# Optimization experiments

Measured on AMD Instinct MI355X. Metric: run time of the kernel, lower is better.

## Reference

```python
import jax, jax.numpy as jnp
import numpy as np

H = 16  # num_heads


def setup_inputs() -> dict:
    key = jax.random.key(0)
    ks = jax.random.split(key, 8)
    B, S, d, L = 1, 2048, 1024, 8
    hd = d // H
    s = 0.02
    return {
        "x": jax.random.normal(ks[0], (B, S, d), jnp.float32),
        "past_values": jax.random.normal(ks[1], (L, B, H, S, hd), jnp.float32),
        "Wqkv": jax.random.normal(ks[2], (3 * d, d), jnp.float32) * s,
        "bqkv": jax.random.normal(ks[3], (3 * d,), jnp.float32) * s,
        "Wcol": jax.random.normal(ks[4], (d, d), jnp.float32) * s,
        "bcol": jax.random.normal(ks[5], (d,), jnp.float32) * s,
        "Wout": jax.random.normal(ks[6], (d, d), jnp.float32) * s,
        "bout": jax.random.normal(ks[7], (d,), jnp.float32) * s,
    }


def reference(x, past_values, Wqkv, bqkv, Wcol, bcol, Wout, bout):
    B, S, d = x.shape
    L = past_values.shape[0]
    hd = d // H
    scale = 1.0 / np.sqrt(hd).astype(np.float32)

    qkv = x @ Wqkv.T + bqkv                       # [B,S,3d]
    q, k, v = jnp.split(qkv, 3, axis=-1)

    def heads(t):                                  # [B,S,d] -> [B,H,S,hd]
        return t.reshape(B, S, H, hd).transpose(0, 2, 1, 3)

    q_row, k, v = heads(q), heads(k), heads(v)
    q_col = heads(x @ Wcol.T + bcol)

    # causal token scores [B,H,S,S]
    token_scores = jnp.einsum('bhqd,bhkd->bhqk', q_row, k) * scale
    causal = jnp.triu(jnp.ones((S, S), bool), 1)
    token_scores = jnp.where(causal, -jnp.inf, token_scores)

    # stack past values: torch stack(dim=3) -> [B,H,S,L,hd]; permute -> [B,S,L,H*hd]
    pv = past_values.transpose(1, 3, 0, 2, 4).reshape(B, S, L, d)
    ri = pv.reshape(B, S * L, d)
    mu = ri.mean(-1, keepdims=True)
    var = ri.var(-1, keepdims=True)
    ri = (ri - mu) / jnp.sqrt(var + 1e-5)          # F.layer_norm, no affine

    Wk, bk = Wqkv[d:2 * d], bqkv[d:2 * d]
    Wv, bv = Wqkv[2 * d:], bqkv[2 * d:]
    rk = (ri @ Wk.T + bk).reshape(B, S * L, H, hd).transpose(0, 2, 1, 3).reshape(B, H, S, L, hd)
    rv = (ri @ Wv.T + bv).reshape(B, S * L, H, hd).transpose(0, 2, 1, 3).reshape(B, H, S, L, hd)

    mem_scores = jnp.einsum('bhsd,bhsld->bhsl', q_col, rk) * scale  # [B,H,S,L]

    scores = jnp.concatenate([token_scores, mem_scores], axis=-1)   # [B,H,S,S+L]
    w = jax.nn.softmax(scores, axis=-1)
    tw, mw = w[..., :S], w[..., S:]

    ctx = jnp.einsum('bhqk,bhkd->bhqd', tw, v) + jnp.einsum('bhsl,bhsld->bhsd', mw, rv)
    out = ctx.transpose(0, 2, 1, 3).reshape(B, S, d)
    return out @ Wout.T + bout
```

## Files before the change

### kernel.cpp

```cpp
#include <hip/hip_runtime.h>
#include <math.h>

#define D   1024
#define H   16
#define HD  64
#define SEQ 2048
#define LL  8
#define SCALE 0.125f

typedef __attribute__((ext_vector_type(8))) __bf16 bf16x8;
typedef __attribute__((ext_vector_type(4))) float floatx4;
typedef __attribute__((ext_vector_type(8))) unsigned short ushort8;

__device__ inline unsigned short f32_to_bf16(float f) {
    unsigned int u = __builtin_bit_cast(unsigned int, f);
    u += 0x7FFF + ((u >> 16) & 1);
    return (unsigned short)(u >> 16);
}
__device__ inline float bf2f(unsigned short u) {
    unsigned int x = (unsigned int)u << 16;
    return __builtin_bit_cast(float, x);
}
__device__ inline void load_lds16(const void* g, void* l) {
    __builtin_amdgcn_global_load_lds(
        (__attribute__((address_space(1))) void*)g,
        (__attribute__((address_space(3))) void*)l, 16, 0, 0);
}

__device__ inline void xcd_swizzle(int& bx, int& by) {
    const int gx   = gridDim.x;
    const int lin  = blockIdx.y * gx + blockIdx.x;
    const int nblk = gx * gridDim.y;
    const int virt = (lin & 7) * (nblk >> 3) + (lin >> 3);
    bx = virt % gx;
    by = virt / gx;
}

#define NQ_X    524288
#define NQ_WQKV 786432
#define NQ_WC   262144
#define NQ_WO   262144
#define LN_BLK  16384
#define CVT_BLK 7168
#define PREP_GRID (LN_BLK + CVT_BLK + 4)

__global__ __launch_bounds__(256) void prep_kernel(
    const float* __restrict__ pv, const float* __restrict__ x,
    const float* __restrict__ Wqkv, const float* __restrict__ Wcol,
    const float* __restrict__ Wout, const float* __restrict__ bqkv,
    const float* __restrict__ bcol,
    unsigned short* __restrict__ ri, unsigned short* __restrict__ xb,
    unsigned short* __restrict__ W4b, unsigned short* __restrict__ Woutb,
    float* __restrict__ b4)
{
    const int b = blockIdx.x;
    const int t = threadIdx.x;
    if (b < LN_BLK) {
        const int r = b;
        const int s = r >> 3, l = r & 7;
        const int h = t >> 4, e = (t & 15) * 4;
        const size_t src = (size_t)l * (H * SEQ * HD) + (size_t)h * (SEQ * HD)
                         + (size_t)s * HD + e;
        float4 v = *(const float4*)(pv + src);
        float sum = v.x + v.y + v.z + v.w;
        float sq  = v.x * v.x + v.y * v.y + v.z * v.z + v.w * v.w;
#pragma unroll
        for (int off = 32; off; off >>= 1) {
            sum += __shfl_xor(sum, off);
            sq  += __shfl_xor(sq, off);
        }
        __shared__ float red[8];
        if ((t & 63) == 0) { red[(t >> 6) * 2] = sum; red[(t >> 6) * 2 + 1] = sq; }
        __syncthreads();
        sum = red[0] + red[2] + red[4] + red[6];
        sq  = red[1] + red[3] + red[5] + red[7];
        const float mean = sum * (1.f / 1024.f);
        const float var  = sq * (1.f / 1024.f) - mean * mean;
        const float rstd = rsqrtf(var + 1e-5f);
        ushort4 o;
        o.x = f32_to_bf16((v.x - mean) * rstd);
        o.y = f32_to_bf16((v.y - mean) * rstd);
        o.z = f32_to_bf16((v.z - mean) * rstd);
        o.w = f32_to_bf16((v.w - mean) * rstd);
        *(ushort4*)(ri + (size_t)r * D + t * 4) = o;
    } else if (b < LN_BLK + CVT_BLK) {
        const int i = (b - LN_BLK) * 256 + t;
        const float* src; unsigned short* dst; int off;
        if (i < NQ_X)                        { src = x;    dst = xb;    off = i; }
        else if (i < NQ_X + NQ_WQKV)         { src = Wqkv; dst = W4b;   off = i - NQ_X; }
        else if (i < NQ_X + NQ_WQKV + NQ_WC) {
            float4 v = ((const float4*)Wcol)[i - NQ_X - NQ_WQKV];
            ushort4 o;
            o.x = f32_to_bf16(v.x); o.y = f32_to_bf16(v.y);
            o.z = f32_to_bf16(v.z); o.w = f32_to_bf16(v.w);
            ((ushort4*)(W4b))[NQ_WQKV + (i - NQ_X - NQ_WQKV)] = o;
            return;
        }
        else                                 { src = Wout; dst = Woutb; off = i - NQ_X - NQ_WQKV - NQ_WC; }
        float4 v = ((const float4*)src)[off];
        ushort4 o;
        o.x = f32_to_bf16(v.x); o.y = f32_to_bf16(v.y);
        o.z = f32_to_bf16(v.z); o.w = f32_to_bf16(v.w);
        ((ushort4*)dst)[off] = o;
    } else {
        const int q = (b - LN_BLK - CVT_BLK) * 256 + t;
        float4 v = (q < 768) ? ((const float4*)bqkv)[q] : ((const float4*)bcol)[q - 768];
        ((float4*)b4)[q] = v;
    }
}

__global__ __launch_bounds__(256) void wkt_kernel(
    const float* __restrict__ Wqkv, unsigned short* __restrict__ WkT)
{
    const int h = blockIdx.x >> 4, ct = blockIdx.x & 15;
    const int c0 = ct * 64;
    const int t = threadIdx.x;
    __shared__ float tile[64][68];
    {
        const int e  = t >> 2;
        const int c4 = (t & 3) * 16;
        const float* src = Wqkv + (size_t)(D + h * HD + e) * D + c0 + c4;
#pragma unroll
        for (int j = 0; j < 4; j++) {
            float4 v = ((const float4*)src)[j];
            *(float4*)&tile[e][c4 + j * 4] = v;
        }
    }
    __syncthreads();
    {
        const int c  = t >> 2;
        const int e0 = (t & 3) * 16;
        ushort8 o0, o1;
#pragma unroll
        for (int j = 0; j < 8; j++) o0[j] = f32_to_bf16(tile[e0 + j][c]);
#pragma unroll
        for (int j = 0; j < 8; j++) o1[j] = f32_to_bf16(tile[e0 + 8 + j][c]);
        unsigned short* dst = WkT + (size_t)h * (D * HD) + (size_t)(c0 + c) * HD + e0;
        *(ushort8*)dst       = o0;
        *(ushort8*)(dst + 8) = o1;
    }
}

template <typename CT, bool HAS_BIAS>
__global__ __launch_bounds__(256) void gemm_bf16_kernel(
    const unsigned short* __restrict__ A, const unsigned short* __restrict__ W,
    const float* __restrict__ bias, CT* __restrict__ C,
    int K, int N, int lda, int ldw, int ldc,
    size_t zsA, size_t zsW, size_t zsC)
{
    A += (size_t)blockIdx.z * zsA;
    W += (size_t)blockIdx.z * zsW;
    C += (size_t)blockIdx.z * zsC;

    __shared__ unsigned short As[128 * 32];
    __shared__ unsigned short Ws[128 * 32];
    const int t    = threadIdx.x;
    const int wave = t >> 6, lane = t & 63;
    const int wm   = wave >> 1, wn = wave & 1;
    int bx, by;
    xcd_swizzle(bx, by);
    const int m0 = by * 128, n0 = bx * 128;

    floatx4 acc[4][4];
#pragma unroll
    for (int i = 0; i < 4; i++)
#pragma unroll
        for (int j = 0; j < 4; j++) acc[i][j] = (floatx4)0.f;

    const int lrow = lane >> 2;
    const int lcol = (lane & 3) * 8;
    const unsigned short* Ag = A + (size_t)(m0 + wave * 32 + lrow) * lda + lcol;
    const unsigned short* Wg = W + (size_t)(n0 + wave * 32 + lrow) * ldw + lcol;
    unsigned short* Asw = &As[wave * 32 * 32];
    unsigned short* Wsw = &Ws[wave * 32 * 32];
    const size_t rowskipA = (size_t)16 * lda;
    const size_t rowskipW = (size_t)16 * ldw;

    const int arow  = lane & 15;
    const int aquad = (lane >> 4) * 8;

    for (int k0 = 0; k0 < K; k0 += 32) {
        load_lds16(Ag + k0,             Asw);
        load_lds16(Ag + k0 + rowskipA,  Asw + 16 * 32);
        load_lds16(Wg + k0,             Wsw);
        load_lds16(Wg + k0 + rowskipW,  Wsw + 16 * 32);
        __syncthreads();

        bf16x8 af[4], wf[4];
#pragma unroll
        for (int mi = 0; mi < 4; mi++)
            af[mi] = *(const bf16x8*)&As[(wm * 64 + mi * 16 + arow) * 32 + aquad];
#pragma unroll
        for (int ni = 0; ni < 4; ni++)
            wf[ni] = *(const bf16x8*)&Ws[(wn * 64 + ni * 16 + arow) * 32 + aquad];
#pragma unroll
        for (int mi = 0; mi < 4; mi++)
#pragma unroll
            for (int ni = 0; ni < 4; ni++)
                acc[mi][ni] = __builtin_amdgcn_mfma_f32_16x16x32_bf16(
                    af[mi], wf[ni], acc[mi][ni], 0, 0, 0);
        __syncthreads();
    }

    const int crow = (lane >> 4) * 4, ccol = lane & 15;
#pragma unroll
    for (int mi = 0; mi < 4; mi++) {
#pragma unroll
        for (int ni = 0; ni < 4; ni++) {
            const int gm = m0 + wm * 64 + mi * 16 + crow;
            const int gn = n0 + wn * 64 + ni * 16 + ccol;
            float bb = 0.f;
            if constexpr (HAS_BIAS) bb = bias[gn];
#pragma unroll
            for (int r = 0; r < 4; r++) {
                float v = acc[mi][ni][r] + bb;
                if constexpr (sizeof(CT) == 2)
                    C[(size_t)(gm + r) * ldc + gn] = (CT)f32_to_bf16(v);
                else
                    C[(size_t)(gm + r) * ldc + gn] = v;
            }
        }
    }
}

#define RI_STRIDE 1032

__global__ __launch_bounds__(256) void memsc_kernel(
    const unsigned short* __restrict__ U, const unsigned short* __restrict__ ri,
    const unsigned short* __restrict__ qkv4, const float* __restrict__ bqkv,
    float* __restrict__ scores)
{
    const int s = blockIdx.x;
    const int t = threadIdx.x;
    __shared__ unsigned short riS[LL * RI_STRIDE];
    __shared__ float qbS[H];
    {
        const unsigned short* src = ri + (size_t)s * (LL * D);
#pragma unroll
        for (int j = 0; j < 4; j++) {
            const int off = (j * 256 + t) * 8;
            const int l = off >> 10, c = off & 1023;
            ushort8 v = *(const ushort8*)(src + off);
            *(ushort8*)&riS[l * RI_STRIDE + c] = v;
        }
    }
    {
        const int h = t >> 4, sub = t & 15;
        const unsigned short* qc = qkv4 + (size_t)s * 4096 + 3 * D + h * HD + sub * 4;
        const float* bk = bqkv + D + h * HD + sub * 4;
        float acc = 0.f;
#pragma unroll
        for (int j = 0; j < 4; j++) acc += bf2f(qc[j]) * bk[j];
#pragma unroll
        for (int off = 1; off < 16; off <<= 1) acc += __shfl_xor(acc, off);
        if (sub == 0) qbS[h] = acc;
    }
    __syncthreads();
    const int p = t >> 1, half = t & 1;
    const int h = p >> 3, l = p & 7;
    const unsigned short* Up = U + ((size_t)h * SEQ + s) * D + half * 512;
    const unsigned short* rp = &riS[l * RI_STRIDE + half * 512];
    float acc = 0.f;
#pragma unroll 4
    for (int j = 0; j < 64; j++) {
        ushort8 u = *(const ushort8*)(Up + j * 8);
        ushort8 r = *(const ushort8*)(rp + j * 8);
#pragma unroll
        for (int k = 0; k < 8; k++) acc += bf2f(u[k]) * bf2f(r[k]);
    }
    acc += __shfl_xor(acc, 1);
    if (half == 0)
        scores[((size_t)s * H + h) * LL + l] = (acc + qbS[h]) * SCALE;
}

__global__ __launch_bounds__(256) void attn_split_kernel(
    const unsigned short* __restrict__ qkv4,
    const float* __restrict__ mem_scores, float* __restrict__ memP,
    float* __restrict__ Opart, float2* __restrict__ mlpart)
{
    const int t    = threadIdx.x;
    const int w    = t >> 6, lane = t & 63;
    const int lrow = lane & 15;
    const int lk   = (lane >> 4) * 8;
    const int rrow = (lane >> 4) * 4;
    const int lin  = blockIdx.x;
    const int hsp  = lin & 63, g = lin >> 6;
    const int h    = hsp >> 2, s = hsp & 3;
    const int qt   = 31 - g;
    const int q0   = qt * 64;
    const int n    = qt + 1;
    const int lo   = (s * n) >> 2, hi = ((s + 1) * n) >> 2;
    const int part = (h * 32 + qt) * 4 + s;

    __shared__ unsigned short Ks[64 * 72];
    __shared__ unsigned short Vt[64 * 72];
    __shared__ unsigned short Pb[64 * 72];
    __shared__ float row_m[64], row_l[64];
    __shared__ float mem_mm[64], mem_alpha[64], mem_suml[64];

    bf16x8 qreg[2];
#pragma unroll
    for (int kst = 0; kst < 2; kst++)
        qreg[kst] = *(const bf16x8*)(qkv4 + (size_t)(q0 + w * 16 + lrow) * 4096
                                     + h * HD + kst * 32 + lk);

    bf16x8 kr[2];
    ushort8 va, vb;
    const int vpr = t & 31, veg = t >> 5;

    float m_i[4], l_i[4];
    floatx4 Oacc[4];
#pragma unroll
    for (int r = 0; r < 4; r++) { m_i[r] = -1e30f; l_i[r] = 0.f; }
#pragma unroll
    for (int et = 0; et < 4; et++) Oacc[et] = (floatx4)0.f;

    const int krow = (t >> 3);
    const int kcol = (t & 7) * 8;

    if (lo < hi) {
        const int j0 = lo * 64;
#pragma unroll
        for (int p = 0; p < 2; p++)
            kr[p] = *(const bf16x8*)(qkv4 + (size_t)(j0 + p * 32 + krow) * 4096
                                     + D + h * HD + kcol);
        const unsigned short* v0 =
            qkv4 + (size_t)(j0 + 2 * vpr) * 4096 + 2 * D + h * HD + veg * 8;
        va = *(const ushort8*)v0;
        vb = *(const ushort8*)(v0 + 4096);
#pragma unroll
        for (int p = 0; p < 2; p++)
            *(bf16x8*)&Ks[(p * 32 + krow) * 72 + kcol] = kr[p];
#pragma unroll
        for (int j = 0; j < 8; j++) {
            unsigned int pk = (unsigned int)va[j] | ((unsigned int)vb[j] << 16);
            *(unsigned int*)&Vt[(veg * 8 + j) * 72 + 2 * vpr] = pk;
        }
        __syncthreads();
    }

    for (int jt = lo; jt < hi; jt++) {
        const int j0 = jt * 64;
        const bool pf = (jt + 1 < hi);
        if (pf) {
            const int j0n = (jt + 1) * 64;
#pragma unroll
            for (int p = 0; p < 2; p++)
                kr[p] = *(const bf16x8*)(qkv4 + (size_t)(j0n + p * 32 + krow) * 4096
                                         + D + h * HD + kcol);
            const unsigned short* v0 =
                qkv4 + (size_t)(j0n + 2 * vpr) * 4096 + 2 * D + h * HD + veg * 8;
            va = *(const ushort8*)v0;
            vb = *(const ushort8*)(v0 + 4096);
        }

        floatx4 S[4];
#pragma unroll
        for (int nt = 0; nt < 4; nt++) S[nt] = (floatx4)0.f;
        __builtin_amdgcn_s_setprio(1);
#pragma unroll
        for (int kst = 0; kst < 2; kst++) {
#pragma unroll
            for (int nt = 0; nt < 4; nt++) {
                bf16x8 bk = *(const bf16x8*)&Ks[(nt * 16 + lrow) * 72 + kst * 32 + lk];
                S[nt] = __builtin_amdgcn_mfma_f32_16x16x32_bf16(qreg[kst], bk, S[nt], 0, 0, 0);
            }
        }
        __builtin_amdgcn_s_setprio(0);

        if (j0 != q0) {
#pragma unroll
            for (int r = 0; r < 4; r++) {
                float sc[4];
#pragma unroll
                for (int nt = 0; nt < 4; nt++) sc[nt] = S[nt][r] * SCALE;
                float mx = fmaxf(fmaxf(sc[0], sc[1]), fmaxf(sc[2], sc[3]));
#pragma unroll
                for (int off = 1; off < 16; off <<= 1)
                    mx = fmaxf(mx, __shfl_xor(mx, off));
                const bool keep = __all(mx <= m_i[r] + 8.f);
                const float newm = keep ? m_i[r] : fmaxf(m_i[r], mx);
                float ps = 0.f;
#pragma unroll
                for (int nt = 0; nt < 4; nt++) {
                    float pe = __expf(sc[nt] - newm);
                    ps += pe;
                    Pb[(w * 16 + rrow + r) * 72 + nt * 16 + lrow] = f32_to_bf16(pe);
                }
#pragma unroll
                for (int off = 1; off < 16; off <<= 1)
                    ps += __shfl_xor(ps, off);
                if (keep) {
                    l_i[r] += ps;
                } else {
                    const float alpha = __expf(m_i[r] - newm);
                    m_i[r] = newm;
                    l_i[r] = l_i[r] * alpha + ps;
#pragma unroll
                    for (int et = 0; et < 4; et++) Oacc[et][r] *= alpha;
                }
            }
        } else {
#pragma unroll
            for (int r = 0; r < 4; r++) {
                const int qg = q0 + w * 16 + rrow + r;
                float sc[4];
                float mx = -1e30f;
#pragma unroll
                for (int nt = 0; nt < 4; nt++) {
                    sc[nt] = S[nt][r] * SCALE;
                    if (j0 + nt * 16 + lrow > qg) sc[nt] = -1e30f;
                    mx = fmaxf(mx, sc[nt]);
                }
#pragma unroll
                for (int off = 1; off < 16; off <<= 1)
                    mx = fmaxf(mx, __shfl_xor(mx, off));
                const float newm  = fmaxf(m_i[r], mx);
                const float alpha = __expf(m_i[r] - newm);
                m_i[r] = newm;
                float ps = 0.f;
#pragma unroll
                for (int nt = 0; nt < 4; nt++) {
                    float pe = __expf(sc[nt] - newm);
                    ps += pe;
                    Pb[(w * 16 + rrow + r) * 72 + nt * 16 + lrow] = f32_to_bf16(pe);
                }
#pragma unroll
                for (int off = 1; off < 16; off <<= 1)
                    ps += __shfl_xor(ps, off);
                l_i[r] = l_i[r] * alpha + ps;
#pragma unroll
                for (int et = 0; et < 4; et++) Oacc[et][r] *= alpha;
            }
        }

        __builtin_amdgcn_s_setprio(1);
#pragma unroll
        for (int kst = 0; kst < 2; kst++) {
            bf16x8 ap = *(const bf16x8*)&Pb[(w * 16 + lrow) * 72 + kst * 32 + lk];
#pragma unroll
            for (int et = 0; et < 4; et++) {
                bf16x8 bv = *(const bf16x8*)&Vt[(et * 16 + lrow) * 72 + kst * 32 + lk];
                Oacc[et] = __builtin_amdgcn_mfma_f32_16x16x32_bf16(ap, bv, Oacc[et], 0, 0, 0);
            }
        }
        __builtin_amdgcn_s_setprio(0);

        if (pf) {
            __syncthreads();
#pragma unroll
            for (int p = 0; p < 2; p++)
                *(bf16x8*)&Ks[(p * 32 + krow) * 72 + kcol] = kr[p];
#pragma unroll
            for (int j = 0; j < 8; j++) {
                unsigned int pk = (unsigned int)va[j] | ((unsigned int)vb[j] << 16);
                *(unsigned int*)&Vt[(veg * 8 + j) * 72 + 2 * vpr] = pk;
            }
            __syncthreads();
        }
    }

    if (s != 0) {
#pragma unroll
        for (int r = 0; r < 4; r++) {
            const int ql = w * 16 + rrow + r;
            if (lrow == 0) mlpart[(size_t)part * 64 + ql] = make_float2(m_i[r], l_i[r]);
#pragma unroll
            for (int et = 0; et < 4; et++)
                Opart[((size_t)part * 64 + ql) * 64 + et * 16 + lrow] = Oacc[et][r];
        }
        return;
    }

#pragma unroll
    for (int r = 0; r < 4; r++) {
        const int ql = w * 16 + rrow + r;
        if (lrow == 0) { row_m[ql] = m_i[r]; row_l[ql] = l_i[r]; }
    }
    __syncthreads();

    if (t < 64) {
        const int qi = t, qg = q0 + qi;
        const float* msp = mem_scores + ((size_t)qg * H + h) * LL;
        float ms[LL];
#pragma unroll
        for (int l = 0; l < LL; l++) ms[l] = msp[l];
        const float mo = row_m[qi];
        float mm = mo;
#pragma unroll
        for (int l = 0; l < LL; l++) mm = fmaxf(mm, ms[l]);
        const float alpha = __expf(mo - mm);
        float suml = 0.f;
        float* mp = memP + ((size_t)qg * H + h) * LL;
#pragma unroll
        for (int l = 0; l < LL; l++) {
            float pe = __expf(ms[l] - mm);
            suml += pe;
            mp[l] = pe;
        }
        mem_mm[qi] = mm; mem_alpha[qi] = alpha; mem_suml[qi] = suml;
    }
    __syncthreads();

#pragma unroll
    for (int r = 0; r < 4; r++) {
        const int ql = w * 16 + rrow + r;
        const float alpha = mem_alpha[ql];
        if (lrow == 0)
            mlpart[(size_t)part * 64 + ql] =
                make_float2(mem_mm[ql], l_i[r] * alpha + mem_suml[ql]);
#pragma unroll
        for (int et = 0; et < 4; et++)
            Opart[((size_t)part * 64 + ql) * 64 + et * 16 + lrow] = Oacc[et][r] * alpha;
    }
}

__global__ __launch_bounds__(256) void attn_merge_kernel(
    const float* __restrict__ Opart, const float2* __restrict__ mlpart,
    const float* __restrict__ memP,
    float* __restrict__ tok, float* __restrict__ mwf, float* __restrict__ Pmem)
{
    const int blk = blockIdx.x;
    const int h = blk >> 5, qt = blk & 31;
    const int q0 = qt * 64;
    const int t = threadIdx.x, tx = t & 15, ty = t >> 4;
    const size_t pb = (size_t)blk * 4;
#pragma unroll
    for (int i = 0; i < 4; i++) {
        const int qi = ty * 4 + i, qg = q0 + qi;
        float2 ml[4];
#pragma unroll
        for (int ps = 0; ps < 4; ps++) ml[ps] = mlpart[(pb + ps) * 64 + qi];
        float M = ml[0].x;
#pragma unroll
        for (int ps = 1; ps < 4; ps++) M = fmaxf(M, ml[ps].x);
        float f[4], L = 0.f;
#pragma unroll
        for (int ps = 0; ps < 4; ps++) { f[ps] = __expf(ml[ps].x - M); L += ml[ps].y * f[ps]; }
        const float rl = 1.f / L;
        float4 o = make_float4(0.f, 0.f, 0.f, 0.f);
#pragma unroll
        for (int ps = 0; ps < 4; ps++) {
            const float fs = f[ps] * rl;
            float4 op = *(const float4*)&Opart[((pb + ps) * 64 + qi) * 64 + tx * 4];
            o.x += op.x * fs; o.y += op.y * fs; o.z += op.z * fs; o.w += op.w * fs;
        }
        *(float4*)&tok[(size_t)qg * D + h * HD + tx * 4] = o;
        if (tx == 0) {
            const float w0 = f[0] * rl;
            const float* mp = memP + ((size_t)qg * H + h) * LL;
            float* mw = mwf + ((size_t)qg * H + h) * LL;
            float psum = 0.f;
#pragma unroll
            for (int l = 0; l < LL; l++) { float v = mp[l] * w0; mw[l] = v; psum += v; }
            Pmem[(size_t)qg * H + h] = psum;
        }
    }
}

__global__ __launch_bounds__(256) void rbar_kernel(
    const float* __restrict__ mwf, const unsigned short* __restrict__ ri,
    unsigned short* __restrict__ rbar)
{
    const int s = blockIdx.x, t = threadIdx.x;
    __shared__ unsigned short riS[LL * D];
    __shared__ float wS[H * LL];
    {
        const unsigned short* src = ri + (size_t)s * (LL * D);
#pragma unroll
        for (int j = 0; j < 4; j++) {
            const int off = (j * 256 + t) * 8;
            *(ushort8*)&riS[off] = *(const ushort8*)(src + off);
        }
    }
    if (t < H * LL) wS[t] = mwf[(size_t)s * (H * LL) + t];
    __syncthreads();
    const int c4 = t * 4;
#pragma unroll
    for (int hh = 0; hh < H; hh++) {
        float v0 = 0.f, v1 = 0.f, v2 = 0.f, v3 = 0.f;
#pragma unroll
        for (int l = 0; l < LL; l++) {
            const float wv = wS[hh * LL + l];
            ushort4 rr = *(const ushort4*)&riS[l * D + c4];
            v0 += wv * bf2f(rr.x); v1 += wv * bf2f(rr.y);
            v2 += wv * bf2f(rr.z); v3 += wv * bf2f(rr.w);
        }
        ushort4 o;
        o.x = f32_to_bf16(v0); o.y = f32_to_bf16(v1);
        o.z = f32_to_bf16(v2); o.w = f32_to_bf16(v3);
        *(ushort4*)(rbar + ((size_t)hh * SEQ + s) * D + c4) = o;
    }
}

__global__ __launch_bounds__(256) void gemm_ctx_kernel(
    const unsigned short* __restrict__ rbar, const unsigned short* __restrict__ W4,
    const float* __restrict__ bqkv, const float* __restrict__ Pmem,
    const float* __restrict__ tok, unsigned short* __restrict__ ctx)
{
    const int mt = blockIdx.x;
    const int h  = blockIdx.y;
    const unsigned short* A  = rbar + (size_t)h * SEQ * D + (size_t)mt * 128 * D;
    const unsigned short* Wv = W4 + (size_t)(2 * D + h * HD) * D;
    const float* bv = bqkv + 2 * D + h * HD;

    __shared__ unsigned short As[128 * 32];
    __shared__ unsigned short Ws[64 * 32];
    const int t    = threadIdx.x;
    const int wave = t >> 6, lane = t & 63;

    floatx4 acc[2][4];
#pragma unroll
    for (int i = 0; i < 2; i++)
#pragma unroll
        for (int j = 0; j < 4; j++) acc[i][j] = (floatx4)0.f;

    const int lrow = lane >> 2;
    const int lcol = (lane & 3) * 8;
    const unsigned short* Ag = A  + (size_t)(wave * 32 + lrow) * D + lcol;
    const unsigned short* Wg = Wv + (size_t)(wave * 32 + lrow) * D + lcol;
    unsigned short* Asw = &As[wave * 32 * 32];
    unsigned short* Wsw = &Ws[wave * 32 * 32];
    const size_t rowskip = (size_t)16 * D;

    const int arow  = lane & 15;
    const int aquad = (lane >> 4) * 8;

    for (int k0 = 0; k0 < D; k0 += 32) {
        load_lds16(Ag + k0,           Asw);
        load_lds16(Ag + k0 + rowskip, Asw + 16 * 32);
        if (wave < 2) {
            load_lds16(Wg + k0,           Wsw);
            load_lds16(Wg + k0 + rowskip, Wsw + 16 * 32);
        }
        __syncthreads();

        bf16x8 af[2], wf[4];
#pragma unroll
        for (int mi = 0; mi < 2; mi++)
            af[mi] = *(const bf16x8*)&As[(wave * 32 + mi * 16 + arow) * 32 + aquad];
#pragma unroll
        for (int ni = 0; ni < 4; ni++)
            wf[ni] = *(const bf16x8*)&Ws[(ni * 16 + arow) * 32 + aquad];
#pragma unroll
        for (int mi = 0; mi < 2; mi++)
#pragma unroll
            for (int ni = 0; ni < 4; ni++)
                acc[mi][ni] = __builtin_amdgcn_mfma_f32_16x16x32_bf16(
                    af[mi], wf[ni], acc[mi][ni], 0, 0, 0);
        __syncthreads();
    }

    const int crow = (lane >> 4) * 4, ccol = lane & 15;
#pragma unroll
    for (int mi = 0; mi < 2; mi++) {
#pragma unroll
        for (int ni = 0; ni < 4; ni++) {
            const int e  = ni * 16 + ccol;
            const float bb = bv[e];
#pragma unroll
            for (int r = 0; r < 4; r++) {
                const int grow = mt * 128 + wave * 32 + mi * 16 + crow + r;
                float v = acc[mi][ni][r] + bb * Pmem[(size_t)grow * H + h]
                          + tok[(size_t)grow * D + h * HD + e];
                ctx[(size_t)grow * D + h * HD + e] = f32_to_bf16(v);
            }
        }
    }
}

extern "C" void kernel_launch(void* const* d_in, const int* in_sizes, int n_in,
                              void* d_out, int out_size, void* d_ws, size_t ws_size,
                              hipStream_t stream)
{
    const float* x    = (const float*)d_in[0];
    const float* pv   = (const float*)d_in[1];
    const float* Wqkv = (const float*)d_in[2];
    const float* bqkv = (const float*)d_in[3];
    const float* Wcol = (const float*)d_in[4];
    const float* bcol = (const float*)d_in[5];
    const float* Wout = (const float*)d_in[6];
    const float* bout = (const float*)d_in[7];
    float* out = (float*)d_out;

    char* p = (char*)d_ws;
    unsigned short* x_bf    = (unsigned short*)p; p += (size_t)2048 * 1024 * 2;
    unsigned short* W4_bf   = (unsigned short*)p; p += (size_t)4096 * 1024 * 2;
    unsigned short* Wout_bf = (unsigned short*)p; p += (size_t)1024 * 1024 * 2;
    float*          b4      = (float*)p;          p += (size_t)4096 * 4;
    unsigned short* ri_bf   = (unsigned short*)p; p += (size_t)16384 * 1024 * 2;
    unsigned short* qkv4_bf = (unsigned short*)p; p += (size_t)2048 * 4096 * 2;
    unsigned short* WkT_bf  = (unsigned short*)p; p += (size_t)16 * 1024 * 64 * 2;
    float*          scores  = (float*)p;          p += (size_t)2048 * 16 * 8 * 4;
    float*          memP    = (float*)p;          p += (size_t)2048 * 16 * 8 * 4;
    float*          mwf     = (float*)p;          p += (size_t)2048 * 16 * 8 * 4;
    float*          Pmem    = (float*)p;          p += (size_t)2048 * 16 * 4;
    float*          tok     = (float*)p;          p += (size_t)2048 * 1024 * 4;
    unsigned short* ctx_bf  = (unsigned short*)p; p += (size_t)2048 * 1024 * 2;
    float*          Opart   = (float*)p;          p += (size_t)2048 * 64 * 64 * 4;
    float2*         mlpart  = (float2*)p;         p += (size_t)2048 * 64 * 8;
    unsigned short* Urb     = (unsigned short*)p; p += (size_t)16 * 2048 * 1024 * 2;

    prep_kernel<<<PREP_GRID, 256, 0, stream>>>(pv, x, Wqkv, Wcol, Wout, bqkv, bcol,
                                               ri_bf, x_bf, W4_bf, Wout_bf, b4);
    wkt_kernel<<<256, 256, 0, stream>>>(Wqkv, WkT_bf);
    gemm_bf16_kernel<unsigned short, true><<<dim3(32, 16, 1), 256, 0, stream>>>(
        x_bf, W4_bf, b4, qkv4_bf, 1024, 4096, 1024, 1024, 4096, 0, 0, 0);
    gemm_bf16_kernel<unsigned short, false><<<dim3(8, 16, 16), 256, 0, stream>>>(
        qkv4_bf + 3 * D, WkT_bf, nullptr, Urb, 64, 1024, 4096, 64, 1024,
        (size_t)HD, (size_t)D * HD, (size_t)SEQ * D);
    memsc_kernel<<<2048, 256, 0, stream>>>(Urb, ri_bf, qkv4_bf, bqkv, scores);
    attn_split_kernel<<<2048, 256, 0, stream>>>(qkv4_bf, scores, memP, Opart, mlpart);
    attn_merge_kernel<<<512, 256, 0, stream>>>(Opart, mlpart, memP, tok, mwf, Pmem);
    rbar_kernel<<<2048, 256, 0, stream>>>(mwf, ri_bf, Urb);
    gemm_ctx_kernel<<<dim3(16, 16), 256, 0, stream>>>(Urb, W4_bf, bqkv, Pmem, tok, ctx_bf);
    gemm_bf16_kernel<float, true><<<dim3(8, 16, 1), 256, 0, stream>>>(
        ctx_bf, Wout_bf, bout, out, 1024, 1024, 1024, 1024, 1024, 0, 0, 0);
}
```

Before: 339.1 us.

## Pre-transpose V and read K/V directly from global in split attention

Adds a kernel that writes V transposed per head into a workspace buffer. The split-attention kernel then reads K and V MFMA operands straight from global memory instead of staging them through shared memory with barriers. Only a per-wave P buffer stays in shared memory. The scale is folded into Q before the bf16 rounding, which slightly changes numerics. The memory-score softmax merge moves from the split kernel into the merge kernel, and the block-to-(head, split) mapping and launch bounds change to raise occupancy. The trade is more uncached global traffic and an extra launch in exchange for no LDS staging and no block-wide syncs.

```diff
diff --git a/kernel.cpp b/kernel.cpp
--- a/kernel.cpp
+++ b/kernel.cpp
@@ -141,6 +141,35 @@
     }
 }
 
+__global__ __launch_bounds__(256) void vtr_kernel(
+    const unsigned short* __restrict__ qkv4, unsigned short* __restrict__ VT)
+{
+    const int h = blockIdx.x & 15, kt = blockIdx.x >> 4;
+    const int t = threadIdx.x;
+    __shared__ unsigned short Vt[64][264];
+    const int pr = t & 31, eg = t >> 5;
+#pragma unroll
+    for (int sub = 0; sub < 4; sub++) {
+        const int j0 = kt * 256 + sub * 64;
+        const unsigned short* v0 = qkv4 + (size_t)(j0 + 2 * pr) * 4096 + 2 * D + h * HD + eg * 8;
+        ushort8 va = *(const ushort8*)v0;
+        ushort8 vb = *(const ushort8*)(v0 + 4096);
+#pragma unroll
+        for (int j = 0; j < 8; j++) {
+            unsigned int pk = (unsigned int)va[j] | ((unsigned int)vb[j] << 16);
+            *(unsigned int*)&Vt[eg * 8 + j][sub * 64 + 2 * pr] = pk;
+        }
+    }
+    __syncthreads();
+#pragma unroll
+    for (int it = 0; it < 8; it++) {
+        const int idx = it * 256 + t;
+        const int e = idx >> 5, ch = idx & 31;
+        ushort8 v = *(const ushort8*)&Vt[e][ch * 8];
+        *(ushort8*)(VT + (size_t)h * (HD * SEQ) + (size_t)e * SEQ + kt * 256 + ch * 8) = v;
+    }
+}
+
 template <typename CT, bool HAS_BIAS>
 __global__ __launch_bounds__(256) void gemm_bf16_kernel(
     const unsigned short* __restrict__ A, const unsigned short* __restrict__ W,
@@ -273,9 +302,8 @@
         scores[((size_t)s * H + h) * LL + l] = (acc + qbS[h]) * SCALE;
 }
 
-__global__ __launch_bounds__(256) void attn_split_kernel(
-    const unsigned short* __restrict__ qkv4,
-    const float* __restrict__ mem_scores, float* __restrict__ memP,
+__global__ __launch_bounds__(256, 4) void attn_split_kernel(
+    const unsigned short* __restrict__ qkv4, const unsigned short* __restrict__ VT,
     float* __restrict__ Opart, float2* __restrict__ mlpart)
 {
     const int t    = threadIdx.x;
@@ -285,28 +313,29 @@
     const int rrow = (lane >> 4) * 4;
     const int lin  = blockIdx.x;
     const int hsp  = lin & 63, g = lin >> 6;
-    const int h    = hsp >> 2, s = hsp & 3;
+    const int s    = hsp >> 4, h = hsp & 15;
     const int qt   = 31 - g;
     const int q0   = qt * 64;
     const int n    = qt + 1;
     const int lo   = (s * n) >> 2, hi = ((s + 1) * n) >> 2;
     const int part = (h * 32 + qt) * 4 + s;
 
-    __shared__ unsigned short Ks[64 * 72];
-    __shared__ unsigned short Vt[64 * 72];
-    __shared__ unsigned short Pb[64 * 72];
-    __shared__ float row_m[64], row_l[64];
-    __shared__ float mem_mm[64], mem_alpha[64], mem_suml[64];
+    __shared__ unsigned short Pb[4][16 * 72];
+    unsigned short* Pw = Pb[w];
 
     bf16x8 qreg[2];
 #pragma unroll
-    for (int kst = 0; kst < 2; kst++)
-        qreg[kst] = *(const bf16x8*)(qkv4 + (size_t)(q0 + w * 16 + lrow) * 4096
-                                     + h * HD + kst * 32 + lk);
-
-    bf16x8 kr[2];
-    ushort8 va, vb;
-    const int vpr = t & 31, veg = t >> 5;
+    for (int kst = 0; kst < 2; kst++) {
+        ushort8 qu = *(const ushort8*)(qkv4 + (size_t)(q0 + w * 16 + lrow) * 4096
+                                       + h * HD + kst * 32 + lk);
+        ushort8 qs;
+#pragma unroll
+        for (int j = 0; j < 8; j++) qs[j] = f32_to_bf16(bf2f(qu[j]) * SCALE);
+        qreg[kst] = __builtin_bit_cast(bf16x8, qs);
+    }
+
+    const unsigned short* Kbase = qkv4 + D + h * HD;
+    const unsigned short* Vbase = VT + (size_t)h * (HD * SEQ);
 
     float m_i[4], l_i[4];
     floatx4 Oacc[4];
@@ -315,44 +344,8 @@
 #pragma unroll
     for (int et = 0; et < 4; et++) Oacc[et] = (floatx4)0.f;
 
-    const int krow = (t >> 3);
-    const int kcol = (t & 7) * 8;
-
-    if (lo < hi) {
-        const int j0 = lo * 64;
-#pragma unroll
-        for (int p = 0; p < 2; p++)
-            kr[p] = *(const bf16x8*)(qkv4 + (size_t)(j0 + p * 32 + krow) * 4096
-                                     + D + h * HD + kcol);
-        const unsigned short* v0 =
-            qkv4 + (size_t)(j0 + 2 * vpr) * 4096 + 2 * D + h * HD + veg * 8;
-        va = *(const ushort8*)v0;
-        vb = *(const ushort8*)(v0 + 4096);
-#pragma unroll
-        for (int p = 0; p < 2; p++)
-            *(bf16x8*)&Ks[(p * 32 + krow) * 72 + kcol] = kr[p];
-#pragma unroll
-        for (int j = 0; j < 8; j++) {
-            unsigned int pk = (unsigned int)va[j] | ((unsigned int)vb[j] << 16);
-            *(unsigned int*)&Vt[(veg * 8 + j) * 72 + 2 * vpr] = pk;
-        }
-        __syncthreads();
-    }
-
     for (int jt = lo; jt < hi; jt++) {
         const int j0 = jt * 64;
-        const bool pf = (jt + 1 < hi);
-        if (pf) {
-            const int j0n = (jt + 1) * 64;
-#pragma unroll
-            for (int p = 0; p < 2; p++)
-                kr[p] = *(const bf16x8*)(qkv4 + (size_t)(j0n + p * 32 + krow) * 4096
-                                         + D + h * HD + kcol);
-            const unsigned short* v0 =
-                qkv4 + (size_t)(j0n + 2 * vpr) * 4096 + 2 * D + h * HD + veg * 8;
-            va = *(const ushort8*)v0;
-            vb = *(const ushort8*)(v0 + 4096);
-        }
 
         floatx4 S[4];
 #pragma unroll
@@ -362,18 +355,19 @@
         for (int kst = 0; kst < 2; kst++) {
 #pragma unroll
             for (int nt = 0; nt < 4; nt++) {
-                bf16x8 bk = *(const bf16x8*)&Ks[(nt * 16 + lrow) * 72 + kst * 32 + lk];
+                bf16x8 bk = *(const bf16x8*)(Kbase
+                    + (size_t)(j0 + nt * 16 + lrow) * 4096 + kst * 32 + lk);
                 S[nt] = __builtin_amdgcn_mfma_f32_16x16x32_bf16(qreg[kst], bk, S[nt], 0, 0, 0);
             }
         }
         __builtin_amdgcn_s_setprio(0);
 
-        if (j0 != q0) {
+        if (jt != qt) {
 #pragma unroll
             for (int r = 0; r < 4; r++) {
                 float sc[4];
 #pragma unroll
-                for (int nt = 0; nt < 4; nt++) sc[nt] = S[nt][r] * SCALE;
+                for (int nt = 0; nt < 4; nt++) sc[nt] = S[nt][r];
                 float mx = fmaxf(fmaxf(sc[0], sc[1]), fmaxf(sc[2], sc[3]));
 #pragma unroll
                 for (int off = 1; off < 16; off <<= 1)
@@ -385,7 +379,7 @@
                 for (int nt = 0; nt < 4; nt++) {
                     float pe = __expf(sc[nt] - newm);
                     ps += pe;
-                    Pb[(w * 16 + rrow + r) * 72 + nt * 16 + lrow] = f32_to_bf16(pe);
+                    Pw[(rrow + r) * 72 + nt * 16 + lrow] = f32_to_bf16(pe);
                 }
 #pragma unroll
                 for (int off = 1; off < 16; off <<= 1)
@@ -408,7 +402,7 @@
                 float mx = -1e30f;
 #pragma unroll
                 for (int nt = 0; nt < 4; nt++) {
-                    sc[nt] = S[nt][r] * SCALE;
+                    sc[nt] = S[nt][r];
                     if (j0 + nt * 16 + lrow > qg) sc[nt] = -1e30f;
                     mx = fmaxf(mx, sc[nt]);
                 }
@@ -423,7 +417,7 @@
                 for (int nt = 0; nt < 4; nt++) {
                     float pe = __expf(sc[nt] - newm);
                     ps += pe;
-                    Pb[(w * 16 + rrow + r) * 72 + nt * 16 + lrow] = f32_to_bf16(pe);
+                    Pw[(rrow + r) * 72 + nt * 16 + lrow] = f32_to_bf16(pe);
                 }
 #pragma unroll
                 for (int off = 1; off < 16; off <<= 1)
@@ -437,87 +431,30 @@
         __builtin_amdgcn_s_setprio(1);
 #pragma unroll
         for (int kst = 0; kst < 2; kst++) {
-            bf16x8 ap = *(const bf16x8*)&Pb[(w * 16 + lrow) * 72 + kst * 32 + lk];
+            bf16x8 ap = *(const bf16x8*)&Pw[lrow * 72 + kst * 32 + lk];
 #pragma unroll
             for (int et = 0; et < 4; et++) {
-                bf16x8 bv = *(const bf16x8*)&Vt[(et * 16 + lrow) * 72 + kst * 32 + lk];
+                bf16x8 bv = *(const bf16x8*)(Vbase
+                    + (size_t)(et * 16 + lrow) * SEQ + j0 + kst * 32 + lk);
                 Oacc[et] = __builtin_amdgcn_mfma_f32_16x16x32_bf16(ap, bv, Oacc[et], 0, 0, 0);
             }
         }
         __builtin_amdgcn_s_setprio(0);
-
-        if (pf) {
-            __syncthreads();
-#pragma unroll
-            for (int p = 0; p < 2; p++)
-                *(bf16x8*)&Ks[(p * 32 + krow) * 72 + kcol] = kr[p];
-#pragma unroll
-            for (int j = 0; j < 8; j++) {
-                unsigned int pk = (unsigned int)va[j] | ((unsigned int)vb[j] << 16);
-                *(unsigned int*)&Vt[(veg * 8 + j) * 72 + 2 * vpr] = pk;
-            }
-            __syncthreads();
-        }
-    }
-
-    if (s != 0) {
-#pragma unroll
-        for (int r = 0; r < 4; r++) {
-            const int ql = w * 16 + rrow + r;
-            if (lrow == 0) mlpart[(size_t)part * 64 + ql] = make_float2(m_i[r], l_i[r]);
-#pragma unroll
-            for (int et = 0; et < 4; et++)
-                Opart[((size_t)part * 64 + ql) * 64 + et * 16 + lrow] = Oacc[et][r];
-        }
-        return;
     }
 
 #pragma unroll
     for (int r = 0; r < 4; r++) {
         const int ql = w * 16 + rrow + r;
-        if (lrow == 0) { row_m[ql] = m_i[r]; row_l[ql] = l_i[r]; }
-    }
-    __syncthreads();
-
-    if (t < 64) {
-        const int qi = t, qg = q0 + qi;
-        const float* msp = mem_scores + ((size_t)qg * H + h) * LL;
-        float ms[LL];
-#pragma unroll
-        for (int l = 0; l < LL; l++) ms[l] = msp[l];
-        const float mo = row_m[qi];
-        float mm = mo;
-#pragma unroll
-        for (int l = 0; l < LL; l++) mm = fmaxf(mm, ms[l]);
-        const float alpha = __expf(mo - mm);
-        float suml = 0.f;
-        float* mp = memP + ((size_t)qg * H + h) * LL;
-#pragma unroll
-        for (int l = 0; l < LL; l++) {
-            float pe = __expf(ms[l] - mm);
-            suml += pe;
-            mp[l] = pe;
-        }
-        mem_mm[qi] = mm; mem_alpha[qi] = alpha; mem_suml[qi] = suml;
-    }
-    __syncthreads();
-
-#pragma unroll
-    for (int r = 0; r < 4; r++) {
-        const int ql = w * 16 + rrow + r;
-        const float alpha = mem_alpha[ql];
-        if (lrow == 0)
-            mlpart[(size_t)part * 64 + ql] =
-                make_float2(mem_mm[ql], l_i[r] * alpha + mem_suml[ql]);
+        if (lrow == 0) mlpart[(size_t)part * 64 + ql] = make_float2(m_i[r], l_i[r]);
 #pragma unroll
         for (int et = 0; et < 4; et++)
-            Opart[((size_t)part * 64 + ql) * 64 + et * 16 + lrow] = Oacc[et][r] * alpha;
+            Opart[((size_t)part * 64 + ql) * 64 + et * 16 + lrow] = Oacc[et][r];
     }
 }
 
 __global__ __launch_bounds__(256) void attn_merge_kernel(
     const float* __restrict__ Opart, const float2* __restrict__ mlpart,
-    const float* __restrict__ memP,
+    const float* __restrict__ scores,
     float* __restrict__ tok, float* __restrict__ mwf, float* __restrict__ Pmem)
 {
     const int blk = blockIdx.x;
@@ -531,12 +468,21 @@
         float2 ml[4];
 #pragma unroll
         for (int ps = 0; ps < 4; ps++) ml[ps] = mlpart[(pb + ps) * 64 + qi];
+        const float* msp = scores + ((size_t)qg * H + h) * LL;
+        float ms[LL];
+#pragma unroll
+        for (int l = 0; l < LL; l++) ms[l] = msp[l];
         float M = ml[0].x;
 #pragma unroll
         for (int ps = 1; ps < 4; ps++) M = fmaxf(M, ml[ps].x);
+#pragma unroll
+        for (int l = 0; l < LL; l++) M = fmaxf(M, ms[l]);
         float f[4], L = 0.f;
 #pragma unroll
         for (int ps = 0; ps < 4; ps++) { f[ps] = __expf(ml[ps].x - M); L += ml[ps].y * f[ps]; }
+        float pm[LL];
+#pragma unroll
+        for (int l = 0; l < LL; l++) { pm[l] = __expf(ms[l] - M); L += pm[l]; }
         const float rl = 1.f / L;
         float4 o = make_float4(0.f, 0.f, 0.f, 0.f);
 #pragma unroll
@@ -547,12 +493,10 @@
         }
         *(float4*)&tok[(size_t)qg * D + h * HD + tx * 4] = o;
         if (tx == 0) {
-            const float w0 = f[0] * rl;
-            const float* mp = memP + ((size_t)qg * H + h) * LL;
             float* mw = mwf + ((size_t)qg * H + h) * LL;
             float psum = 0.f;
 #pragma unroll
-            for (int l = 0; l < LL; l++) { float v = mp[l] * w0; mw[l] = v; psum += v; }
+            for (int l = 0; l < LL; l++) { float v = pm[l] * rl; mw[l] = v; psum += v; }
             Pmem[(size_t)qg * H + h] = psum;
         }
     }
@@ -691,8 +635,8 @@
     unsigned short* ri_bf   = (unsigned short*)p; p += (size_t)16384 * 1024 * 2;
     unsigned short* qkv4_bf = (unsigned short*)p; p += (size_t)2048 * 4096 * 2;
     unsigned short* WkT_bf  = (unsigned short*)p; p += (size_t)16 * 1024 * 64 * 2;
+    unsigned short* VT_bf   = (unsigned short*)p; p += (size_t)16 * 64 * 2048 * 2;
     float*          scores  = (float*)p;          p += (size_t)2048 * 16 * 8 * 4;
-    float*          memP    = (float*)p;          p += (size_t)2048 * 16 * 8 * 4;
     float*          mwf     = (float*)p;          p += (size_t)2048 * 16 * 8 * 4;
     float*          Pmem    = (float*)p;          p += (size_t)2048 * 16 * 4;
     float*          tok     = (float*)p;          p += (size_t)2048 * 1024 * 4;
@@ -706,12 +650,13 @@
     wkt_kernel<<<256, 256, 0, stream>>>(Wqkv, WkT_bf);
     gemm_bf16_kernel<unsigned short, true><<<dim3(32, 16, 1), 256, 0, stream>>>(
         x_bf, W4_bf, b4, qkv4_bf, 1024, 4096, 1024, 1024, 4096, 0, 0, 0);
+    vtr_kernel<<<128, 256, 0, stream>>>(qkv4_bf, VT_bf);
     gemm_bf16_kernel<unsigned short, false><<<dim3(8, 16, 16), 256, 0, stream>>>(
         qkv4_bf + 3 * D, WkT_bf, nullptr, Urb, 64, 1024, 4096, 64, 1024,
         (size_t)HD, (size_t)D * HD, (size_t)SEQ * D);
     memsc_kernel<<<2048, 256, 0, stream>>>(Urb, ri_bf, qkv4_bf, bqkv, scores);
-    attn_split_kernel<<<2048, 256, 0, stream>>>(qkv4_bf, scores, memP, Opart, mlpart);
-    attn_merge_kernel<<<512, 256, 0, stream>>>(Opart, mlpart, memP, tok, mwf, Pmem);
+    attn_split_kernel<<<2048, 256, 0, stream>>>(qkv4_bf, VT_bf, Opart, mlpart);
+    attn_merge_kernel<<<512, 256, 0, stream>>>(Opart, mlpart, scores, tok, mwf, Pmem);
     rbar_kernel<<<2048, 256, 0, stream>>>(mwf, ri_bf, Urb);
     gemm_ctx_kernel<<<dim3(16, 16), 256, 0, stream>>>(Urb, W4_bf, bqkv, Pmem, tok, ctx_bf);
     gemm_bf16_kernel<float, true><<<dim3(8, 16, 1), 256, 0, stream>>>(
```

After: 378.1 us. 1.12x slower.
